# Kernel tuning notes

Measured on AMD Instinct MI355X. Metric: run time of the kernel, lower is better.

The kernel has to match this reference:

```python
import jax, jax.numpy as jnp
import numpy as np

PRIMES = (2, 3, 5, 7, 11, 13, 17, 19, 23, 29)
TEMP = 1000.0  # softmax_temperature
B, S = 32, 2048

def _templates(p):
    # circle template for residue r: (cos(2*pi*r/p), sin(2*pi*r/p)) -> [p, 2]
    ang = 2.0 * np.pi * np.arange(p) / p
    return jnp.asarray(np.stack([np.cos(ang), np.sin(ang)], axis=-1).astype(np.float32))

def _mul_onehot(p):
    # onehot[a, b, (a*b) % p] = 1 -> [p, p, p]
    t = (np.arange(p)[:, None] * np.arange(p)[None, :]) % p
    return jnp.asarray((t[..., None] == np.arange(p)).astype(np.float32))

TEMPLATES = [_templates(p) for p in PRIMES]
MUL_OH = [_mul_onehot(p) for p in PRIMES]

def setup_inputs() -> dict:
    key = jax.random.key(0)
    k1, k2 = jax.random.split(key)
    m = len(PRIMES)
    return {
        "a_circle": jax.random.normal(k1, (B, S, m, 2), dtype=jnp.float32),
        "b_circle": jax.random.normal(k2, (B, S, m, 2), dtype=jnp.float32),
    }

def _circle_add(a, b):
    # complex multiply: angles add -> (a + b) mod p on the circle
    ca, sa = a[..., 0], a[..., 1]
    cb, sb = b[..., 0], b[..., 1]
    return jnp.stack([ca * cb - sa * sb, sa * cb + ca * sb], axis=-1)

def _circle_sub(a, b):
    # a - b = a + conj(b): negate sin of b
    b_conj = jnp.stack([b[..., 0], -b[..., 1]], axis=-1)
    return _circle_add(a, b_conj)

def _decode_soft(c_i, tmpl):
    # c_i: [B, S, 2], tmpl: [p, 2] -> soft one-hot over residues [B, S, p]
    sim = jnp.einsum('bsd,pd->bsp', c_i, tmpl)
    return jax.nn.softmax(TEMP * sim, axis=-1)

def _circle_mul(a, b):
    outs = []
    for i, p in enumerate(PRIMES):
        tmpl = TEMPLATES[i]
        a_soft = _decode_soft(a[:, :, i, :], tmpl)
        b_soft = _decode_soft(b[:, :, i, :], tmpl)
        # outer product of soft residues contracted with mul table
        dist = jnp.einsum('bsi,bsj,ijk->bsk', a_soft, b_soft, MUL_OH[i])
        outs.append(dist @ tmpl)  # re-encode to circle: [B, S, 2]
    return jnp.stack(outs, axis=2)  # [B, S, m, 2]

def reference(a_circle, b_circle):
    add = _circle_add(a_circle, b_circle)
    sub = _circle_sub(a_circle, b_circle)
    mul = _circle_mul(a_circle, b_circle)
    return jnp.stack([add, sub, mul], axis=0)  # [3, B, S, m, 2]
```

## Files before the change

### kernel.cpp

```cpp
#include <hip/hip_runtime.h>


#define SOFTMAX_TEMP 1000.0f

constexpr double PI_D = 3.14159265358979323846264338327950288;

constexpr double tay_cos(double x) {
    double x2 = x * x, term = 1.0, sum = 1.0;
    for (int k = 1; k <= 15; ++k) { term *= -x2 / double((2 * k - 1) * (2 * k)); sum += term; }
    return sum;
}
constexpr double tay_sin(double x) {
    double x2 = x * x, term = x, sum = x;
    for (int k = 1; k <= 15; ++k) { term *= -x2 / double((2 * k) * (2 * k + 1)); sum += term; }
    return sum;
}

template <int P> struct Tab { float c[P]; float s[P]; };

template <int P>
constexpr Tab<P> make_tab() {
    Tab<P> t{};
    for (int r = 0; r < P; ++r) {
        double x = 2.0 * PI_D * double(r) / double(P);
        if (x > PI_D) x -= 2.0 * PI_D;
        t.c[r] = (float)tay_cos(x);
        t.s[r] = (float)tay_sin(x);
    }
    return t;
}

template <int P>
__device__ __forceinline__ void mul_prime(float ca, float sa, float cb, float sb,
                                          float& oc, float& os) {
    constexpr Tab<P> T = make_tab<P>();

    float ma = -1e30f, mb = -1e30f;
#pragma unroll
    for (int r = 0; r < P; ++r) {
        ma = fmaxf(ma, ca * T.c[r] + sa * T.s[r]);
        mb = fmaxf(mb, cb * T.c[r] + sb * T.s[r]);
    }

    float eb[P];
    float Sb = 0.f;
#pragma unroll
    for (int r = 0; r < P; ++r) {
        float x = __expf(SOFTMAX_TEMP * (cb * T.c[r] + sb * T.s[r] - mb));
        eb[r] = x; Sb += x;
    }

    float W[P];
#pragma unroll
    for (int k = 0; k < P; ++k) W[k] = 0.f;

    float Sa = 0.f, ea0 = 0.f;
#pragma unroll
    for (int i = 0; i < P; ++i) {
        float ea_i = __expf(SOFTMAX_TEMP * (ca * T.c[i] + sa * T.s[i] - ma));
        Sa += ea_i;
        if (i == 0) { ea0 = ea_i; }
        else {
#pragma unroll
            for (int j = 1; j < P; ++j) {
                const int k = (i * j) % P;
                W[k] = fmaf(ea_i, eb[j], W[k]);
            }
        }
    }
    W[0] += ea0 * Sb + eb[0] * (Sa - ea0);

    float accC = 0.f, accS = 0.f;
#pragma unroll
    for (int k = 0; k < P; ++k) {
        accC = fmaf(W[k], T.c[k], accC);
        accS = fmaf(W[k], T.s[k], accS);
    }
    const float inv = 1.0f / (Sa * Sb);
    oc = accC * inv;
    os = accS * inv;
}

__global__ __launch_bounds__(640) void arith_kernel(const float* __restrict__ a,
                                                    const float* __restrict__ b,
                                                    float* __restrict__ out,
                                                    int n_pairs) {
    __shared__ float2 t0[64 * 11], t1[64 * 11];
    __shared__ float2 o0[64 * 11], o1[64 * 11], o2[64 * 11];

    const int t = threadIdx.x;
    const int pr = t / 10, of = t - pr * 10;
    const int li = pr * 11 + of;
    const int gf = blockIdx.x * 640 + t;

    t0[li] = ((const float2*)a)[gf];
    t1[li] = ((const float2*)b)[gf];
    __syncthreads();

    const int lane = t & 63;
    const int pi = t >> 6;
    const int lc = lane * 11 + pi;
    const float2 av = t0[lc];
    const float2 bv = t1[lc];
    const float ca = av.x, sa = av.y, cb = bv.x, sb = bv.y;

    const float pcc = ca * cb, pss = sa * sb, psc = sa * cb, pcs = ca * sb;

    float oc, os;
    switch (pi) {
        case 0: mul_prime<2>(ca, sa, cb, sb, oc, os); break;
        case 1: mul_prime<3>(ca, sa, cb, sb, oc, os); break;
        case 2: mul_prime<5>(ca, sa, cb, sb, oc, os); break;
        case 3: mul_prime<7>(ca, sa, cb, sb, oc, os); break;
        case 4: mul_prime<11>(ca, sa, cb, sb, oc, os); break;
        case 5: mul_prime<13>(ca, sa, cb, sb, oc, os); break;
        case 6: mul_prime<17>(ca, sa, cb, sb, oc, os); break;
        case 7: mul_prime<19>(ca, sa, cb, sb, oc, os); break;
        case 8: mul_prime<23>(ca, sa, cb, sb, oc, os); break;
        default: mul_prime<29>(ca, sa, cb, sb, oc, os); break;
    }

    o0[lc] = make_float2(pcc - pss, psc + pcs);
    o1[lc] = make_float2(pcc + pss, psc - pcs);
    o2[lc] = make_float2(oc, os);
    __syncthreads();

    const int planef2 = n_pairs * 10;
    float2* o = (float2*)out;
    o[gf]                = o0[li];
    o[planef2 + gf]      = o1[li];
    o[2 * planef2 + gf]  = o2[li];
}

extern "C" void kernel_launch(void* const* d_in, const int* in_sizes, int n_in,
                              void* d_out, int out_size, void* d_ws, size_t ws_size,
                              hipStream_t stream) {
    const float* a = (const float*)d_in[0];
    const float* b = (const float*)d_in[1];
    float* out = (float*)d_out;
    const int n_pairs = in_sizes[0] / 20;
    const int n_groups = n_pairs / 64;

    dim3 block(640);
    dim3 grid(n_groups);
    arith_kernel<<<grid, block, 0, stream>>>(a, b, out, n_pairs);
}
```

Baseline: 79.91 us.

## Exploit residue symmetry and fold temperature into exp2 templates

Folds the softmax temperature and log2(e) into the similarity templates so each exponent is a raw hardware exp2 with no extra multiply. Uses the r and P-r symmetry of the circle: pairs of exponentials are combined into sum and difference terms, which roughly halves the inner outer-product FMAs and the re-encode loop. Adds a closed-form specialization for P=2. The intent is to cut ALU work in the divergent per-prime mul path; the new form trades exactness of the summation order for fewer operations.

```diff
diff --git a/kernel.cpp b/kernel.cpp
--- a/kernel.cpp
+++ b/kernel.cpp
@@ -1,7 +1,7 @@
 #include <hip/hip_runtime.h>
 
 
-#define SOFTMAX_TEMP 1000.0f
+#define TEMP_LOG2E 1442.6950408889634f
 
 constexpr double PI_D = 3.14159265358979323846264338327950288;
 
@@ -15,17 +15,28 @@
     for (int k = 1; k <= 15; ++k) { term *= -x2 / double((2 * k) * (2 * k + 1)); sum += term; }
     return sum;
 }
+constexpr double ang_red(int r, int P) {
+    double x = 2.0 * PI_D * double(r) / double(P);
+    return (x > PI_D) ? x - 2.0 * PI_D : x;
+}
 
-template <int P> struct Tab { float c[P]; float s[P]; };
-
+template <int P> struct TabS { float c[P]; float s[P]; };
 template <int P>
-constexpr Tab<P> make_tab() {
-    Tab<P> t{};
+constexpr TabS<P> make_tabs() {
+    TabS<P> t{};
     for (int r = 0; r < P; ++r) {
-        double x = 2.0 * PI_D * double(r) / double(P);
-        if (x > PI_D) x -= 2.0 * PI_D;
-        t.c[r] = (float)tay_cos(x);
-        t.s[r] = (float)tay_sin(x);
+        t.c[r] = (float)(double(TEMP_LOG2E) * tay_cos(ang_red(r, P)));
+        t.s[r] = (float)(double(TEMP_LOG2E) * tay_sin(ang_red(r, P)));
+    }
+    return t;
+}
+template <int P> struct TabE { float c[P / 2 + 1]; float s[P / 2 + 1]; };
+template <int P>
+constexpr TabE<P> make_tabe() {
+    TabE<P> t{};
+    for (int k = 0; k <= P / 2; ++k) {
+        t.c[k] = (float)tay_cos(ang_red(k, P));
+        t.s[k] = (float)tay_sin(ang_red(k, P));
     }
     return t;
 }
@@ -33,7 +44,10 @@
 template <int P>
 __device__ __forceinline__ void mul_prime(float ca, float sa, float cb, float sb,
                                           float& oc, float& os) {
-    constexpr Tab<P> T = make_tab<P>();
+    static_assert(P % 2 == 1, "generic path requires odd P");
+    constexpr int H = (P - 1) / 2;
+    constexpr TabS<P> T = make_tabs<P>();
+    constexpr TabE<P> E = make_tabe<P>();
 
     float ma = -1e30f, mb = -1e30f;
 #pragma unroll
@@ -42,43 +56,68 @@
         mb = fmaxf(mb, cb * T.c[r] + sb * T.s[r]);
     }
 
-    float eb[P];
-    float Sb = 0.f;
+    float eb0 = __builtin_amdgcn_exp2f(cb * T.c[0] - mb);
+    float Sb = eb0;
+    float ub[H], vb[H];
 #pragma unroll
-    for (int r = 0; r < P; ++r) {
-        float x = __expf(SOFTMAX_TEMP * (cb * T.c[r] + sb * T.s[r] - mb));
-        eb[r] = x; Sb += x;
+    for (int j = 1; j <= H; ++j) {
+        float e1 = __builtin_amdgcn_exp2f(cb * T.c[j] + sb * T.s[j] - mb);
+        float e2 = __builtin_amdgcn_exp2f(cb * T.c[P - j] + sb * T.s[P - j] - mb);
+        Sb += e1 + e2;
+        ub[j - 1] = e1 + e2;
+        vb[j - 1] = e1 - e2;
     }
 
-    float W[P];
+    float A[H], Bacc[H];
 #pragma unroll
-    for (int k = 0; k < P; ++k) W[k] = 0.f;
+    for (int k = 0; k < H; ++k) { A[k] = 0.f; Bacc[k] = 0.f; }
 
-    float Sa = 0.f, ea0 = 0.f;
+    float ea0 = __builtin_amdgcn_exp2f(ca * T.c[0] - ma);
+    float Sa = ea0;
 #pragma unroll
-    for (int i = 0; i < P; ++i) {
-        float ea_i = __expf(SOFTMAX_TEMP * (ca * T.c[i] + sa * T.s[i] - ma));
-        Sa += ea_i;
-        if (i == 0) { ea0 = ea_i; }
-        else {
+    for (int i = 1; i <= H; ++i) {
+        float f1 = __builtin_amdgcn_exp2f(ca * T.c[i] + sa * T.s[i] - ma);
+        float f2 = __builtin_amdgcn_exp2f(ca * T.c[P - i] + sa * T.s[P - i] - ma);
+        Sa += f1 + f2;
+        const float ua = f1 + f2, va = f1 - f2;
 #pragma unroll
-            for (int j = 1; j < P; ++j) {
-                const int k = (i * j) % P;
-                W[k] = fmaf(ea_i, eb[j], W[k]);
-            }
+        for (int j = 1; j <= H; ++j) {
+            constexpr int dummy = 0; (void)dummy;
+            const int k0 = (i * j) % P;
+            const int kr = (k0 <= H) ? k0 : P - k0;
+            A[kr - 1] = fmaf(ua, ub[j - 1], A[kr - 1]);
+            if (k0 <= H) Bacc[kr - 1] = fmaf(va,  vb[j - 1], Bacc[kr - 1]);
+            else         Bacc[kr - 1] = fmaf(-va, vb[j - 1], Bacc[kr - 1]);
         }
     }
-    W[0] += ea0 * Sb + eb[0] * (Sa - ea0);
 
-    float accC = 0.f, accS = 0.f;
+    const float W0 = ea0 * Sb + eb0 * (Sa - ea0);
+
+    float accC = W0, accS = 0.f;
 #pragma unroll
-    for (int k = 0; k < P; ++k) {
-        accC = fmaf(W[k], T.c[k], accC);
-        accS = fmaf(W[k], T.s[k], accS);
+    for (int k = 1; k <= H; ++k) {
+        accC = fmaf(A[k - 1],    E.c[k], accC);
+        accS = fmaf(Bacc[k - 1], E.s[k], accS);
     }
     const float inv = 1.0f / (Sa * Sb);
     oc = accC * inv;
     os = accS * inv;
+}
+
+template <>
+__device__ __forceinline__ void mul_prime<2>(float ca, float sa, float cb, float sb,
+                                             float& oc, float& os) {
+    const float ka = ca * TEMP_LOG2E, kb = cb * TEMP_LOG2E;
+    const float ma = fabsf(ka), mb = fabsf(kb);
+    const float ea0 = __builtin_amdgcn_exp2f(ka - ma);
+    const float ea1 = __builtin_amdgcn_exp2f(-ka - ma);
+    const float eb0 = __builtin_amdgcn_exp2f(kb - mb);
+    const float eb1 = __builtin_amdgcn_exp2f(-kb - mb);
+    const float Sa = ea0 + ea1, Sb = eb0 + eb1;
+    const float W0 = ea0 * Sb + eb0 * Sa - ea0 * eb0;
+    const float W1 = ea1 * eb1;
+    oc = (W0 - W1) / (Sa * Sb);
+    os = 0.f;
 }
 
 __global__ __launch_bounds__(640) void arith_kernel(const float* __restrict__ a,
@@ -127,9 +166,9 @@
 
     const int planef2 = n_pairs * 10;
     float2* o = (float2*)out;
-    o[gf]                = o0[li];
-    o[planef2 + gf]      = o1[li];
-    o[2 * planef2 + gf]  = o2[li];
+    o[gf]               = o0[li];
+    o[planef2 + gf]     = o1[li];
+    o[2 * planef2 + gf] = o2[li];
 }
 
 extern "C" void kernel_launch(void* const* d_in, const int* in_sizes, int n_in,
```

Result: faster. 75.45 us (-5.6%).
